# Kernel tuning notes

Measured on AMD Instinct MI355X. Metric: run time of the kernel, lower is better.

The kernel has to match this reference:

```python
import jax, jax.numpy as jnp
import numpy as np

# Model dims (match init_kwargs)
D_OUT = 64      # d_in == d_out
SEQ_L = 4096    # input_len
K_EIG = 24      # num_eigh
K_U = 3         # auto_reg_k_u
K_Y = 2         # auto_reg_k_y
BATCH = 8


def get_top_hankel_eigh(n, k):
    """Top-k eigenpairs of the Hankel matrix Z[i,j] = 2/((i+j)^3-(i+j)), 1-indexed."""
    idx = np.arange(1, n + 1, dtype=np.float64)
    s = idx[:, None] + idx[None, :]
    z = 2.0 / (s ** 3 - s)
    vals, vecs = np.linalg.eigh(z)  # ascending
    return (jnp.asarray(vals[-k:], jnp.float32),        # [k]
            jnp.asarray(vecs[:, -k:], jnp.float32))     # [n, k]


def setup_inputs() -> dict:
    key = jax.random.key(0)
    k1, k2, k3, k4 = jax.random.split(key, 4)
    eig_vals, eig_vecs = get_top_hankel_eigh(SEQ_L, K_EIG)
    m_x_var = 1.0 / float(D_OUT) ** 0.5
    return {
        "inputs": jax.random.normal(k1, (BATCH, SEQ_L, D_OUT), jnp.float32),
        "m_y": jax.random.normal(k2, (D_OUT, K_Y, D_OUT), jnp.float32) * 0.01,
        "m_u": jax.random.normal(k3, (D_OUT, D_OUT, K_U), jnp.float32) * m_x_var,
        "m_phi": jax.random.normal(k4, (D_OUT * K_EIG, D_OUT), jnp.float32) * 0.01,
        "eig_vals": eig_vals,
        "eig_vecs": eig_vecs,
    }


def _stu_single(x, m_y, m_u, m_phi, eig_vals, eig_vecs):
    """apply_stu for one sequence x: [L, d] -> [L, d]."""
    L, d = x.shape
    n = 2 * L
    # --- compute_x_tilde: causal FFT conv of each eigenvector with each channel ---
    V = jnp.fft.rfft(eig_vecs, n=n, axis=0)             # [F, k]
    U = jnp.fft.rfft(x, n=n, axis=0)                    # [F, d]
    xt = jnp.fft.irfft(V[:, :, None] * U[:, None, :], n=n, axis=0)[:L]  # [L, k, d]
    xt = xt * (eig_vals ** 0.25)[None, :, None]
    x_tilde = xt.reshape(L, K_EIG * d)                  # [L, k*d]
    # --- delta_phi ---
    delta_phi = jnp.einsum('lk,kd->ld', x_tilde, m_phi)  # [L, d_out]
    # --- compute_ar_x_preds: shifted AR input contributions ---
    o = jnp.einsum('oik,li->klo', m_u, x)               # [k_u, L, d_out]
    shifts = jnp.arange(K_U)
    o = jax.vmap(lambda a, i: jnp.roll(a, i, axis=0))(o, shifts)
    mask = (jnp.arange(L)[None, :] >= shifts[:, None]).astype(x.dtype)  # [k_u, L]
    delta_ar_u = jnp.sum(o * mask[:, :, None], axis=0)  # [L, d_out]
    deltas = delta_phi + delta_ar_u
    # --- compute_y_t: sequential AR recurrence over time ---
    def step(carry, dlt):  # carry: [k_y, d_out]
        out = jnp.tensordot(m_y, carry, axes=2) + dlt    # [d_out]
        carry = jnp.roll(carry, 1, axis=0).at[0].set(out)
        return carry, out
    _, ys = jax.lax.scan(step, jnp.zeros((K_Y, d), x.dtype), deltas)
    return ys  # [L, d_out]


def reference(inputs, m_y, m_u, m_phi, eig_vals, eig_vecs):
    return jax.vmap(lambda x: _stu_single(x, m_y, m_u, m_phi, eig_vals, eig_vecs))(inputs)
```

## Files before the change

kernel.cpp:

```cpp
#include <hip/hip_runtime.h>
#include <math.h>

#define BB 8
#define LL 4096
#define DD 64
#define KK 24
#define KT 27
#define NN 8192
#define LOGN 13
#define NP 4128
#define NCH 256
#define CH 16
#define PAD 80

typedef unsigned int uint;
typedef unsigned short u16;
typedef __attribute__((ext_vector_type(8))) short bf16x8;
typedef __attribute__((ext_vector_type(4))) float f32x4;

__device__ __forceinline__ float bfl(uint u) {
    union { uint u; float f; } v; v.u = u << 16; return v.f;
}
__device__ __forceinline__ float bfh(uint u) {
    union { uint u; float f; } v; v.u = u & 0xFFFF0000u; return v.f;
}
__device__ __forceinline__ uint pk(float x) {
    union { float f; uint u; } v; v.f = x;
    return (v.u + 0x7FFFu + ((v.u >> 16) & 1u)) >> 16;
}
__device__ __forceinline__ float2 unpk2(uint u) {
    return make_float2(bfl(u), bfh(u));
}
__device__ __forceinline__ int br13(int v) { return (int)(__brev((uint)v) >> 19); }

__global__ __launch_bounds__(512) void k_twiddle(float2* __restrict__ twc) {
    int i = blockIdx.x * 512 + threadIdx.x;
    if (i >= 8192) return;
    if (i == 0) { twc[0] = make_float2(1.f, 0.f); return; }
    int lh = 31 - __builtin_clz((uint)i);
    int j = i - (1 << lh);
    float ang = -6.28318530717958647692f * (float)j / (float)(2 << lh);
    float sn, cs;
    __sincosf(ang, &sn, &cs);
    twc[i] = make_float2(cs, sn);
}

template<int NT>
__device__ __forceinline__ void fft_dif(float2* a, const float2* __restrict__ twc) {
    const int tid = threadIdx.x;
    for (int lh = LOGN - 1; lh >= 0; --lh) {
        const int half = 1 << lh;
#pragma unroll
        for (int bb = 0; bb < NN / 2 / NT; ++bb) {
            int t = tid + bb * NT;
            int j = t & (half - 1);
            int i0 = ((t >> lh) << (lh + 1)) + j;
            float2 u = a[i0], v = a[i0 + half];
            float2 w = twc[half + j];
            float cs = w.x, sn = w.y;
            float dx = u.x - v.x, dy = u.y - v.y;
            a[i0] = make_float2(u.x + v.x, u.y + v.y);
            a[i0 + half] = make_float2(dx * cs - dy * sn, dx * sn + dy * cs);
        }
        __syncthreads();
    }
}

template<int NT>
__device__ __forceinline__ void fft_dit(float2* a, const float2* __restrict__ twc) {
    const int tid = threadIdx.x;
    for (int lh = 0; lh < LOGN; ++lh) {
        const int half = 1 << lh;
#pragma unroll
        for (int bb = 0; bb < NN / 2 / NT; ++bb) {
            int t = tid + bb * NT;
            int j = t & (half - 1);
            int i0 = ((t >> lh) << (lh + 1)) + j;
            float2 u = a[i0], v = a[i0 + half];
            float2 w = twc[half + j];
            float cs = w.x, sn = -w.y;
            float wx = v.x * cs - v.y * sn;
            float wy = v.x * sn + v.y * cs;
            a[i0] = make_float2(u.x + wx, u.y + wy);
            a[i0 + half] = make_float2(u.x - wx, u.y - wy);
        }
        __syncthreads();
    }
}


__global__ __launch_bounds__(256) void k_pack(const float* __restrict__ mphi,
                                              const float* __restrict__ mu,
                                              uint* __restrict__ mp2) {
    int idx = blockIdx.x * 256 + threadIdx.x;
    if (idx >= KT * 2048) return;
    int k = idx >> 11;
    int rem = idx & 2047;
    int o = rem >> 5, cp = rem & 31;
    int c = cp * 2;
    uint v;
    if (k < KK) {
        v = pk(mphi[(k * 64 + c) * 64 + o]) | (pk(mphi[(k * 64 + c + 1) * 64 + o]) << 16);
    } else {
        int ku = k - KK;
        v = pk(mu[(o * 64 + c) * 3 + ku]) | (pk(mu[(o * 64 + c + 1) * 3 + ku]) << 16);
    }
    mp2[idx] = v;
}

__global__ __launch_bounds__(256) void k_fft_filters(const float* __restrict__ eig_vals,
                                                     const float* __restrict__ eig_vecs,
                                                     const float2* __restrict__ twc,
                                                     float2* __restrict__ Vb) {
    __shared__ float2 a[NN];
    const int k = blockIdx.x, tid = threadIdx.x;
    const float alpha = powf(eig_vals[k], 0.25f) * (1.0f / (float)NN);
    for (int t = tid; t < LL; t += 256)
        a[t] = make_float2(eig_vecs[t * KK + k] * alpha, 0.f);
    for (int t = LL + tid; t < NN; t += 256)
        a[t] = make_float2(0.f, 0.f);
    __syncthreads();
    fft_dif<256>(a, twc);
    for (int r = tid; r < NN; r += 256)
        Vb[(size_t)r * KK + k] = a[r];
}

__global__ __launch_bounds__(512) void k_fft_x2(const float* __restrict__ x,
                                                const float2* __restrict__ twc,
                                                uint* __restrict__ Uxp,
                                                uint* __restrict__ Uyp) {
    __shared__ float2 a[NN];
    const int b = blockIdx.x & 7, cp = blockIdx.x >> 3;
    const int tid = threadIdx.x;
    for (int l = tid; l < LL; l += 512)
        a[l] = *(const float2*)&x[((size_t)b * LL + l) * DD + 2 * cp];
    for (int l = LL + tid; l < NN; l += 512)
        a[l] = make_float2(0.f, 0.f);
    __syncthreads();
    fft_dif<512>(a, twc);
    const size_t plane = ((size_t)b * 32 + cp) * NP;
    for (int idx = tid; idx < 4097; idx += 512) {
        int r = (idx == 4096) ? 1 : 2 * idx;
        int fn = br13(r);
        int q = br13((8192 - fn) & 8191);
        float2 Z = a[r], W = a[q];
        float ucx = 0.5f * (Z.x + W.x), ucy = 0.5f * (Z.y - W.y);
        float upx = 0.5f * (Z.y + W.y), upy = 0.5f * (W.x - Z.x);
        Uxp[plane + idx] = pk(ucx) | (pk(upx) << 16);
        Uyp[plane + idx] = pk(ucy) | (pk(upy) << 16);
    }
    for (int idx = 4097 + tid; idx < NP; idx += 512) {
        Uxp[plane + idx] = 0;
        Uyp[plane + idx] = 0;
    }
}

__global__ __launch_bounds__(256) void k_modulate5(const float2* __restrict__ Vb,
                                                   const uint* __restrict__ Uxp,
                                                   const uint* __restrict__ Uyp,
                                                   const uint* __restrict__ mp2,
                                                   uint* __restrict__ Sb2) {
    __shared__ u16 Uxs[32][PAD];
    __shared__ u16 Uys[32][PAD];
    __shared__ u16 mpT[2][64][PAD];
    __shared__ float2 Vt[32][28];
    const int tid = threadIdx.x;
    const int pt = blockIdx.x;
    const int b  = blockIdx.y;
    const int p0 = pt * 32;

    for (int i = tid; i < 1024; i += 256) {
        int cp = i >> 5, row = i & 31;
        uint vx = Uxp[((size_t)b * 32 + cp) * NP + p0 + row];
        uint vy = Uyp[((size_t)b * 32 + cp) * NP + p0 + row];
        *(uint*)&Uxs[row][cp * 2] = vx;
        *(uint*)&Uys[row][cp * 2] = vy;
    }
    {
        int o = tid >> 2, seg = tid & 3;
        const uint4* src = (const uint4*)&mp2[(size_t)o * 32 + seg * 8];
        uint4 m0 = src[0], m1 = src[1];
        *(uint4*)&mpT[0][o][seg * 16] = m0;
        *(uint4*)&mpT[0][o][seg * 16 + 8] = m1;
    }
    for (int i = tid; i < 768; i += 256) {
        int pi = i / 24, kk = i - pi * 24;
        int pidx = p0 + pi; if (pidx > 4096) pidx = 4096;
        int r = (pidx == 4096) ? 1 : 2 * pidx;
        Vt[pi][kk] = Vb[(size_t)r * KK + kk];
    }
    for (int pi = tid; pi < 32; pi += 256) {
        int pidx = p0 + pi; if (pidx > 4096) pidx = 4096;
        int r = (pidx == 4096) ? 1 : 2 * pidx;
        int f = br13(r);
        const float invN = 1.f / 8192.f;
        float ph = -6.28318530717958647692f * (float)f * invN;
        float s1, c1, s2, c2;
        __sincosf(ph, &s1, &c1);
        __sincosf(2.f * ph, &s2, &c2);
        Vt[pi][24] = make_float2(invN, 0.f);
        Vt[pi][25] = make_float2(c1 * invN, s1 * invN);
        Vt[pi][26] = make_float2(c2 * invN, s2 * invN);
    }
    __syncthreads();

    const int lane = tid & 63, w = tid >> 6;
    const int rt = w & 1, chalf = w >> 1;
    const int lrow = lane & 15, lk = lane >> 4;
    const u16* axp = &Uxs[rt * 16 + lrow][lk * 8];
    const u16* ayp = &Uys[rt * 16 + lrow][lk * 8];

    float Sx0[4] = {0.f, 0.f, 0.f, 0.f}, Sy0[4] = {0.f, 0.f, 0.f, 0.f};
    float Sx1[4] = {0.f, 0.f, 0.f, 0.f}, Sy1[4] = {0.f, 0.f, 0.f, 0.f};

    for (int k = 0; k < KT; ++k) {
        const int cur = k & 1;
        bf16x8 ax0 = *(const bf16x8*)(axp);
        bf16x8 ax1 = *(const bf16x8*)(axp + 32);
        bf16x8 ay0 = *(const bf16x8*)(ayp);
        bf16x8 ay1 = *(const bf16x8*)(ayp + 32);
        const u16* bp0 = &mpT[cur][chalf * 32 + lrow][lk * 8];
        const u16* bp1 = &mpT[cur][chalf * 32 + 16 + lrow][lk * 8];
        bf16x8 b00 = *(const bf16x8*)(bp0);
        bf16x8 b01 = *(const bf16x8*)(bp0 + 32);
        bf16x8 b10 = *(const bf16x8*)(bp1);
        bf16x8 b11 = *(const bf16x8*)(bp1 + 32);
        float2 v0 = Vt[rt * 16 + lk * 4 + 0][k];
        float2 v1 = Vt[rt * 16 + lk * 4 + 1][k];
        float2 v2 = Vt[rt * 16 + lk * 4 + 2][k];
        float2 v3 = Vt[rt * 16 + lk * 4 + 3][k];
        if (k + 1 < KT) {
            int o = tid >> 2, seg = tid & 3;
            const uint4* src = (const uint4*)&mp2[((size_t)(k + 1) * 64 + o) * 32 + seg * 8];
            uint4 m0 = src[0], m1 = src[1];
            *(uint4*)&mpT[cur ^ 1][o][seg * 16] = m0;
            *(uint4*)&mpT[cur ^ 1][o][seg * 16 + 8] = m1;
        }
        f32x4 z = {0.f, 0.f, 0.f, 0.f};
        f32x4 Wx0 = __builtin_amdgcn_mfma_f32_16x16x32_bf16(ax0, b00, z, 0, 0, 0);
        Wx0 = __builtin_amdgcn_mfma_f32_16x16x32_bf16(ax1, b01, Wx0, 0, 0, 0);
        f32x4 Wy0 = __builtin_amdgcn_mfma_f32_16x16x32_bf16(ay0, b00, z, 0, 0, 0);
        Wy0 = __builtin_amdgcn_mfma_f32_16x16x32_bf16(ay1, b01, Wy0, 0, 0, 0);
        f32x4 Wx1 = __builtin_amdgcn_mfma_f32_16x16x32_bf16(ax0, b10, z, 0, 0, 0);
        Wx1 = __builtin_amdgcn_mfma_f32_16x16x32_bf16(ax1, b11, Wx1, 0, 0, 0);
        f32x4 Wy1 = __builtin_amdgcn_mfma_f32_16x16x32_bf16(ay0, b10, z, 0, 0, 0);
        Wy1 = __builtin_amdgcn_mfma_f32_16x16x32_bf16(ay1, b11, Wy1, 0, 0, 0);
        Sx0[0] += v0.x * Wx0[0] - v0.y * Wy0[0];  Sy0[0] += v0.x * Wy0[0] + v0.y * Wx0[0];
        Sx0[1] += v1.x * Wx0[1] - v1.y * Wy0[1];  Sy0[1] += v1.x * Wy0[1] + v1.y * Wx0[1];
        Sx0[2] += v2.x * Wx0[2] - v2.y * Wy0[2];  Sy0[2] += v2.x * Wy0[2] + v2.y * Wx0[2];
        Sx0[3] += v3.x * Wx0[3] - v3.y * Wy0[3];  Sy0[3] += v3.x * Wy0[3] + v3.y * Wx0[3];
        Sx1[0] += v0.x * Wx1[0] - v0.y * Wy1[0];  Sy1[0] += v0.x * Wy1[0] + v0.y * Wx1[0];
        Sx1[1] += v1.x * Wx1[1] - v1.y * Wy1[1];  Sy1[1] += v1.x * Wy1[1] + v1.y * Wx1[1];
        Sx1[2] += v2.x * Wx1[2] - v2.y * Wy1[2];  Sy1[2] += v2.x * Wy1[2] + v2.y * Wx1[2];
        Sx1[3] += v3.x * Wx1[3] - v3.y * Wy1[3];  Sy1[3] += v3.x * Wy1[3] + v3.y * Wx1[3];
        __syncthreads();
    }
    const int rbase = rt * 16 + lk * 4;
    const int o0 = chalf * 32 + lrow;
    const size_t pl0 = ((size_t)b * 64 + o0) * NP + p0 + rbase;
    const size_t pl1 = ((size_t)b * 64 + o0 + 16) * NP + p0 + rbase;
#pragma unroll
    for (int j = 0; j < 4; ++j) {
        Sb2[pl0 + j] = pk(Sx0[j]) | (pk(Sy0[j]) << 16);
        Sb2[pl1 + j] = pk(Sx1[j]) | (pk(Sy1[j]) << 16);
    }
}

__global__ __launch_bounds__(512) void k_ifft2(const uint* __restrict__ Sb2,
                                               const float2* __restrict__ twc,
                                               float* __restrict__ deltas) {
    __shared__ float2 a[NN];
    const int b = blockIdx.x & 7, op = blockIdx.x >> 3;
    const int tid = threadIdx.x;
    const uint* s0 = &Sb2[((size_t)b * 64 + op * 2) * NP];
    const uint* s1 = &Sb2[((size_t)b * 64 + op * 2 + 1) * NP];
    for (int idx = tid; idx < 4097; idx += 512) {
        int r = (idx == 4096) ? 1 : 2 * idx;
        float2 A = unpk2(s0[idx]), B = unpk2(s1[idx]);
        a[r] = make_float2(A.x - B.y, A.y + B.x);
        int fn = br13(r);
        int q = br13((8192 - fn) & 8191);
        if (q != r) a[q] = make_float2(A.x + B.y, B.x - A.y);
    }
    __syncthreads();
    fft_dit<512>(a, twc);
    float* d0 = &deltas[((size_t)b * 64 + op * 2) * LL];
    float* d1 = &deltas[((size_t)b * 64 + op * 2 + 1) * LL];
    for (int l = tid; l < LL; l += 512) {
        d0[l] = a[l].x;
        d1[l] = a[l].y;
    }
}

__global__ __launch_bounds__(256) void k_matsq1(const float* __restrict__ m_y,
                                                float* __restrict__ C) {
    int idx = blockIdx.x * 256 + threadIdx.x;
    int r = idx >> 7, c = idx & 127;
    if (r >= 64) { C[idx] = m_y[(r - 64) * 128 + c]; return; }
    float acc = (c < 64) ? m_y[r * 128 + 64 + c] : 0.f;
#pragma unroll
    for (int i = 0; i < 64; ++i) acc += m_y[r * 128 + i] * m_y[i * 128 + c];
    C[idx] = acc;
}

__global__ __launch_bounds__(256) void k_matsq(const float* __restrict__ A,
                                               float* __restrict__ C) {
    int idx = blockIdx.x * 256 + threadIdx.x;
    int r = idx >> 7, c = idx & 127;
    float acc = 0.f;
#pragma unroll
    for (int i = 0; i < 128; ++i) acc += A[r * 128 + i] * A[i * 128 + c];
    C[idx] = acc;
}

__device__ __forceinline__ void load_rowhalf(const float* __restrict__ P, int r, int h,
                                             float* __restrict__ p) {
#pragma unroll
    for (int i4 = 0; i4 < 16; ++i4) {
        float4 v = *(const float4*)&P[r * 128 + h * 64 + i4 * 4];
        p[4 * i4] = v.x; p[4 * i4 + 1] = v.y; p[4 * i4 + 2] = v.z; p[4 * i4 + 3] = v.w;
    }
}
__device__ __forceinline__ float dot64(const float* __restrict__ p, const float* s) {
    float a0 = 0.f, a1 = 0.f, a2 = 0.f, a3 = 0.f;
#pragma unroll
    for (int i4 = 0; i4 < 16; ++i4) {
        float4 w = *(const float4*)&s[i4 * 4];
        a0 += p[4 * i4] * w.x;  a1 += p[4 * i4 + 1] * w.y;
        a2 += p[4 * i4 + 2] * w.z;  a3 += p[4 * i4 + 3] * w.w;
    }
    return (a0 + a1) + (a2 + a3);
}

__global__ __launch_bounds__(256, 1) void k_scan(const float* __restrict__ P,
                                                 const float* __restrict__ in,
                                                 float* __restrict__ partial,
                                                 float* __restrict__ terminal,
                                                 const int count) {
    const int bx = blockIdx.x;
    const int tid = threadIdx.x;
    const int r = tid & 127, h = tid >> 7;
    __shared__ __align__(16) float scur[128];
    __shared__ float pacc[256];
    float p[64];
    load_rowhalf(P, r, h, p);
    if (tid < 128) scur[tid] = 0.f;
    __syncthreads();
    const size_t base = (size_t)bx * count * 128;
    for (int k = 0; k < count; ++k) {
        if (tid < 128) partial[base + (size_t)k * 128 + tid] = scur[tid];
        pacc[tid] = dot64(p, &scur[h * 64]);
        __syncthreads();
        if (tid < 128) scur[tid] = pacc[tid] + pacc[tid + 128] + in[base + (size_t)k * 128 + tid];
        __syncthreads();
    }
    if (tid < 128) terminal[(size_t)bx * 128 + tid] = scur[tid];
}

__global__ __launch_bounds__(256, 1) void k_fixupg(const float* __restrict__ P,
                                                   const float* __restrict__ Sinit,
                                                   const float* __restrict__ q,
                                                   float* __restrict__ out,
                                                   const int count) {
    const int bx = blockIdx.x;
    const int tid = threadIdx.x;
    const int r = tid & 127, h = tid >> 7;
    __shared__ __align__(16) float scur[128];
    __shared__ float pacc[256];
    float p[64];
    load_rowhalf(P, r, h, p);
    if (tid < 128) scur[tid] = Sinit[(size_t)bx * 128 + tid];
    __syncthreads();
    const size_t base = (size_t)bx * count * 128;
    for (int k = 0; k < count; ++k) {
        if (tid < 128) out[base + (size_t)k * 128 + tid] = scur[tid] + q[base + (size_t)k * 128 + tid];
        if (k == count - 1) break;
        pacc[tid] = dot64(p, &scur[h * 64]);
        __syncthreads();
        if (tid < 128) scur[tid] = pacc[tid] + pacc[tid + 128];
        __syncthreads();
    }
}

__global__ __launch_bounds__(128, 1) void k_chunk_local(const float* __restrict__ deltas,
                                                        const float* __restrict__ m_y,
                                                        float* __restrict__ term) {
    const int b = blockIdx.x >> 8, j = blockIdx.x & 255;
    const int tid = threadIdx.x;
    const int o = tid & 63, h = tid >> 6;
    __shared__ __align__(16) float y1s[64];
    __shared__ __align__(16) float y2s[64];
    __shared__ float pacc[128];
    float m1[32], m2[32];
#pragma unroll
    for (int i4 = 0; i4 < 8; ++i4) {
        float4 v1 = *(const float4*)&m_y[o * 128 + h * 32 + i4 * 4];
        float4 v2 = *(const float4*)&m_y[o * 128 + 64 + h * 32 + i4 * 4];
        m1[4 * i4] = v1.x; m1[4 * i4 + 1] = v1.y; m1[4 * i4 + 2] = v1.z; m1[4 * i4 + 3] = v1.w;
        m2[4 * i4] = v2.x; m2[4 * i4 + 1] = v2.y; m2[4 * i4 + 2] = v2.z; m2[4 * i4 + 3] = v2.w;
    }
    if (tid < 64) { y1s[tid] = 0.f; y2s[tid] = 0.f; }
    __syncthreads();
    const float* dl = &deltas[((size_t)b * 64 + o) * LL + j * CH];
    for (int t = 0; t < CH; ++t) {
        float a0 = 0.f, a1 = 0.f, a2 = 0.f, a3 = 0.f;
#pragma unroll
        for (int i4 = 0; i4 < 8; ++i4) {
            float4 w1 = *(const float4*)&y1s[h * 32 + i4 * 4];
            float4 w2 = *(const float4*)&y2s[h * 32 + i4 * 4];
            a0 += m1[4 * i4] * w1.x + m2[4 * i4] * w2.x;
            a1 += m1[4 * i4 + 1] * w1.y + m2[4 * i4 + 1] * w2.y;
            a2 += m1[4 * i4 + 2] * w1.z + m2[4 * i4 + 2] * w2.z;
            a3 += m1[4 * i4 + 3] * w1.w + m2[4 * i4 + 3] * w2.w;
        }
        pacc[tid] = (a0 + a1) + (a2 + a3);
        __syncthreads();
        if (h == 0) {
            float outv = pacc[o] + pacc[o + 64] + dl[t];
            y2s[o] = y1s[o];
            y1s[o] = outv;
        }
        __syncthreads();
    }
    if (tid < 64) {
        term[((size_t)b * NCH + j) * 128 + o] = y1s[o];
        term[((size_t)b * NCH + j) * 128 + 64 + o] = y2s[o];
    }
}

__global__ __launch_bounds__(128, 1) void k_chunk_final(const float* __restrict__ deltas,
                                                        const float* __restrict__ m_y,
                                                        const float* __restrict__ sstate,
                                                        float* __restrict__ out) {
    const int b = blockIdx.x >> 8, j = blockIdx.x & 255;
    const int tid = threadIdx.x;
    const int o = tid & 63, h = tid >> 6;
    __shared__ __align__(16) float y1s[64];
    __shared__ __align__(16) float y2s[64];
    __shared__ float pacc[128];
    float m1[32], m2[32];
#pragma unroll
    for (int i4 = 0; i4 < 8; ++i4) {
        float4 v1 = *(const float4*)&m_y[o * 128 + h * 32 + i4 * 4];
        float4 v2 = *(const float4*)&m_y[o * 128 + 64 + h * 32 + i4 * 4];
        m1[4 * i4] = v1.x; m1[4 * i4 + 1] = v1.y; m1[4 * i4 + 2] = v1.z; m1[4 * i4 + 3] = v1.w;
        m2[4 * i4] = v2.x; m2[4 * i4 + 1] = v2.y; m2[4 * i4 + 2] = v2.z; m2[4 * i4 + 3] = v2.w;
    }
    if (tid < 64) {
        y1s[tid] = sstate[((size_t)b * NCH + j) * 128 + tid];
        y2s[tid] = sstate[((size_t)b * NCH + j) * 128 + 64 + tid];
    }
    __syncthreads();
    const float* dl = &deltas[((size_t)b * 64 + o) * LL + j * CH];
    const size_t obase = (((size_t)b * LL) + j * CH) * DD + o;
    for (int t = 0; t < CH; ++t) {
        float a0 = 0.f, a1 = 0.f, a2 = 0.f, a3 = 0.f;
#pragma unroll
        for (int i4 = 0; i4 < 8; ++i4) {
            float4 w1 = *(const float4*)&y1s[h * 32 + i4 * 4];
            float4 w2 = *(const float4*)&y2s[h * 32 + i4 * 4];
            a0 += m1[4 * i4] * w1.x + m2[4 * i4] * w2.x;
            a1 += m1[4 * i4 + 1] * w1.y + m2[4 * i4 + 1] * w2.y;
            a2 += m1[4 * i4 + 2] * w1.z + m2[4 * i4 + 2] * w2.z;
            a3 += m1[4 * i4 + 3] * w1.w + m2[4 * i4 + 3] * w2.w;
        }
        pacc[tid] = (a0 + a1) + (a2 + a3);
        __syncthreads();
        if (h == 0) {
            float outv = pacc[o] + pacc[o + 64] + dl[t];
            out[obase + (size_t)t * DD] = outv;
            y2s[o] = y1s[o];
            y1s[o] = outv;
        }
        __syncthreads();
    }
}

extern "C" void kernel_launch(void* const* d_in, const int* in_sizes, int n_in,
                              void* d_out, int out_size, void* d_ws, size_t ws_size,
                              hipStream_t stream) {
    const float* x        = (const float*)d_in[0];
    const float* m_y      = (const float*)d_in[1];
    const float* m_u      = (const float*)d_in[2];
    const float* m_phi    = (const float*)d_in[3];
    const float* eig_vals = (const float*)d_in[4];
    const float* eig_vecs = (const float*)d_in[5];
    float* out = (float*)d_out;

    char* ws = (char*)d_ws;
    size_t off = 0;
    auto alloc = [&](size_t bytes) -> void* {
        void* p = ws + off;
        off += (bytes + 255) & ~(size_t)255;
        return p;
    };
    float2* Vb   = (float2*)alloc((size_t)NN * KK * sizeof(float2));
    uint*   Uxp  = (uint*)alloc((size_t)BB * 32 * NP * sizeof(uint));
    uint*   Uyp  = (uint*)alloc((size_t)BB * 32 * NP * sizeof(uint));
    uint*   Sb2  = (uint*)alloc((size_t)BB * 64 * NP * sizeof(uint));
    float*  deltas = (float*)alloc((size_t)BB * 64 * LL * sizeof(float));
    uint*   mp2  = (uint*)alloc((size_t)KT * 64 * 32 * sizeof(uint));
    float2* twcg = (float2*)alloc((size_t)8192 * sizeof(float2));
    float*  mats = (float*)alloc((size_t)4 * 128 * 128 * sizeof(float));
    float*  term = (float*)alloc((size_t)BB * NCH * 128 * sizeof(float));
    float*  sst  = (float*)alloc((size_t)BB * NCH * 128 * sizeof(float));
    float*  qbuf = (float*)alloc((size_t)BB * NCH * 128 * sizeof(float));
    float*  Qg   = (float*)alloc((size_t)BB * 16 * 128 * sizeof(float));
    float*  Sgt  = (float*)alloc((size_t)BB * 16 * 128 * sizeof(float));
    float*  dmy  = (float*)alloc((size_t)8 * 128 * sizeof(float));

    k_twiddle<<<dim3(16), dim3(512), 0, stream>>>(twcg);
    k_pack<<<dim3(216), dim3(256), 0, stream>>>(m_phi, m_u, mp2);
    k_fft_filters<<<dim3(24), dim3(256), 0, stream>>>(eig_vals, eig_vecs, twcg, Vb);
    k_fft_x2<<<dim3(256), dim3(512), 0, stream>>>(x, twcg, Uxp, Uyp);

    float* T1   = mats;
    float* T2   = mats + 16384;
    float* P16  = mats + 32768;
    float* P256 = mats + 49152;
    k_matsq1<<<dim3(64), dim3(256), 0, stream>>>(m_y, T1);
    k_matsq<<<dim3(64), dim3(256), 0, stream>>>(T1, T2);
    k_matsq<<<dim3(64), dim3(256), 0, stream>>>(T2, T1);
    k_matsq<<<dim3(64), dim3(256), 0, stream>>>(T1, P16);
    k_matsq<<<dim3(64), dim3(256), 0, stream>>>(P16, T1);
    k_matsq<<<dim3(64), dim3(256), 0, stream>>>(T1, T2);
    k_matsq<<<dim3(64), dim3(256), 0, stream>>>(T2, T1);
    k_matsq<<<dim3(64), dim3(256), 0, stream>>>(T1, P256);

    k_modulate5<<<dim3(129, 8), dim3(256), 0, stream>>>(Vb, Uxp, Uyp, mp2, Sb2);
    k_ifft2<<<dim3(256), dim3(512), 0, stream>>>(Sb2, twcg, deltas);

    k_chunk_local<<<dim3(2048), dim3(128), 0, stream>>>(deltas, m_y, term);
    k_scan<<<dim3(128), dim3(256), 0, stream>>>(P16, term, qbuf, Qg, 16);
    k_scan<<<dim3(8), dim3(256), 0, stream>>>(P256, Qg, Sgt, dmy, 16);
    k_fixupg<<<dim3(128), dim3(256), 0, stream>>>(P16, Sgt, qbuf, sst, 16);
    k_chunk_final<<<dim3(2048), dim3(128), 0, stream>>>(deltas, m_y, sst, out);
}
```

Before: 240.7 us.

## Split modulation into two launches with whole weight slabs preloaded into LDS

The modulation kernel is split into two launches, each covering about half of the 27 weight slabs. Each launch loads all of its slabs into shared memory up front, which removes the per-iteration __syncthreads and double-buffered refill. The U fragments are also hoisted out of the loop. The cost is larger LDS usage (about 143 KB per block, likely one block per CU), a second launch, and a bf16 read-modify-write of Sb2 that adds rounding error and extra global traffic.

New measurement: 315.6 us. 31.1% more time.

```diff
diff --git a/kernel.cpp b/kernel.cpp
--- a/kernel.cpp
+++ b/kernel.cpp
@@ -12,6 +12,7 @@
 #define NCH 256
 #define CH 16
 #define PAD 80
+#define NKMAX 14
 
 typedef unsigned int uint;
 typedef unsigned short u16;
@@ -155,20 +156,28 @@
     }
 }
 
-__global__ __launch_bounds__(256) void k_modulate5(const float2* __restrict__ Vb,
+__global__ __launch_bounds__(256) void k_modulate7(const float2* __restrict__ Vb,
                                                    const uint* __restrict__ Uxp,
                                                    const uint* __restrict__ Uyp,
                                                    const uint* __restrict__ mp2,
-                                                   uint* __restrict__ Sb2) {
-    __shared__ u16 Uxs[32][PAD];
-    __shared__ u16 Uys[32][PAD];
-    __shared__ u16 mpT[2][64][PAD];
-    __shared__ float2 Vt[32][28];
+                                                   uint* __restrict__ Sb2,
+                                                   const int k0, const int nk,
+                                                   const int accum) {
+    __shared__ u16 mpT[NKMAX][64][PAD];
+    __shared__ u16 Uxs[32][72];
+    __shared__ u16 Uys[32][72];
+    __shared__ float2 Vt[32][NKMAX];
     const int tid = threadIdx.x;
     const int pt = blockIdx.x;
     const int b  = blockIdx.y;
     const int p0 = pt * 32;
 
+    for (int i = tid; i < nk * 512; i += 256) {
+        int slab = i >> 9, e = i & 511;
+        int o = e >> 3, seg = e & 7;
+        uint4 m = ((const uint4*)&mp2[((size_t)(k0 + slab) * 64 + o) * 32])[seg];
+        *(uint4*)&mpT[slab][o][seg * 8] = m;
+    }
     for (int i = tid; i < 1024; i += 256) {
         int cp = i >> 5, row = i & 31;
         uint vx = Uxp[((size_t)b * 32 + cp) * NP + p0 + row];
@@ -176,31 +185,21 @@
         *(uint*)&Uxs[row][cp * 2] = vx;
         *(uint*)&Uys[row][cp * 2] = vy;
     }
-    {
-        int o = tid >> 2, seg = tid & 3;
-        const uint4* src = (const uint4*)&mp2[(size_t)o * 32 + seg * 8];
-        uint4 m0 = src[0], m1 = src[1];
-        *(uint4*)&mpT[0][o][seg * 16] = m0;
-        *(uint4*)&mpT[0][o][seg * 16 + 8] = m1;
-    }
-    for (int i = tid; i < 768; i += 256) {
-        int pi = i / 24, kk = i - pi * 24;
+    for (int i = tid; i < 32 * nk; i += 256) {
+        int pi = i / nk, kk = i - pi * nk;
+        int kg = k0 + kk;
         int pidx = p0 + pi; if (pidx > 4096) pidx = 4096;
         int r = (pidx == 4096) ? 1 : 2 * pidx;
-        Vt[pi][kk] = Vb[(size_t)r * KK + kk];
-    }
-    for (int pi = tid; pi < 32; pi += 256) {
-        int pidx = p0 + pi; if (pidx > 4096) pidx = 4096;
-        int r = (pidx == 4096) ? 1 : 2 * pidx;
-        int f = br13(r);
-        const float invN = 1.f / 8192.f;
-        float ph = -6.28318530717958647692f * (float)f * invN;
-        float s1, c1, s2, c2;
-        __sincosf(ph, &s1, &c1);
-        __sincosf(2.f * ph, &s2, &c2);
-        Vt[pi][24] = make_float2(invN, 0.f);
-        Vt[pi][25] = make_float2(c1 * invN, s1 * invN);
-        Vt[pi][26] = make_float2(c2 * invN, s2 * invN);
+        if (kg < KK) {
+            Vt[pi][kk] = Vb[(size_t)r * KK + kg];
+        } else {
+            int f = br13(r);
+            const float invN = 1.f / 8192.f;
+            float ph = -6.28318530717958647692f * (float)f * invN * (float)(kg - KK);
+            float sn, cs;
+            __sincosf(ph, &sn, &cs);
+            Vt[pi][kk] = make_float2(cs * invN, sn * invN);
+        }
     }
     __syncthreads();
 
@@ -209,33 +208,25 @@
     const int lrow = lane & 15, lk = lane >> 4;
     const u16* axp = &Uxs[rt * 16 + lrow][lk * 8];
     const u16* ayp = &Uys[rt * 16 + lrow][lk * 8];
+    bf16x8 ax0 = *(const bf16x8*)(axp);
+    bf16x8 ax1 = *(const bf16x8*)(axp + 32);
+    bf16x8 ay0 = *(const bf16x8*)(ayp);
+    bf16x8 ay1 = *(const bf16x8*)(ayp + 32);
 
     float Sx0[4] = {0.f, 0.f, 0.f, 0.f}, Sy0[4] = {0.f, 0.f, 0.f, 0.f};
     float Sx1[4] = {0.f, 0.f, 0.f, 0.f}, Sy1[4] = {0.f, 0.f, 0.f, 0.f};
 
-    for (int k = 0; k < KT; ++k) {
-        const int cur = k & 1;
-        bf16x8 ax0 = *(const bf16x8*)(axp);
-        bf16x8 ax1 = *(const bf16x8*)(axp + 32);
-        bf16x8 ay0 = *(const bf16x8*)(ayp);
-        bf16x8 ay1 = *(const bf16x8*)(ayp + 32);
-        const u16* bp0 = &mpT[cur][chalf * 32 + lrow][lk * 8];
-        const u16* bp1 = &mpT[cur][chalf * 32 + 16 + lrow][lk * 8];
+    for (int kk = 0; kk < nk; ++kk) {
+        const u16* bp0 = &mpT[kk][chalf * 32 + lrow][lk * 8];
+        const u16* bp1 = &mpT[kk][chalf * 32 + 16 + lrow][lk * 8];
         bf16x8 b00 = *(const bf16x8*)(bp0);
         bf16x8 b01 = *(const bf16x8*)(bp0 + 32);
         bf16x8 b10 = *(const bf16x8*)(bp1);
         bf16x8 b11 = *(const bf16x8*)(bp1 + 32);
-        float2 v0 = Vt[rt * 16 + lk * 4 + 0][k];
-        float2 v1 = Vt[rt * 16 + lk * 4 + 1][k];
-        float2 v2 = Vt[rt * 16 + lk * 4 + 2][k];
-        float2 v3 = Vt[rt * 16 + lk * 4 + 3][k];
-        if (k + 1 < KT) {
-            int o = tid >> 2, seg = tid & 3;
-            const uint4* src = (const uint4*)&mp2[((size_t)(k + 1) * 64 + o) * 32 + seg * 8];
-            uint4 m0 = src[0], m1 = src[1];
-            *(uint4*)&mpT[cur ^ 1][o][seg * 16] = m0;
-            *(uint4*)&mpT[cur ^ 1][o][seg * 16 + 8] = m1;
-        }
+        float2 v0 = Vt[rt * 16 + lk * 4 + 0][kk];
+        float2 v1 = Vt[rt * 16 + lk * 4 + 1][kk];
+        float2 v2 = Vt[rt * 16 + lk * 4 + 2][kk];
+        float2 v3 = Vt[rt * 16 + lk * 4 + 3][kk];
         f32x4 z = {0.f, 0.f, 0.f, 0.f};
         f32x4 Wx0 = __builtin_amdgcn_mfma_f32_16x16x32_bf16(ax0, b00, z, 0, 0, 0);
         Wx0 = __builtin_amdgcn_mfma_f32_16x16x32_bf16(ax1, b01, Wx0, 0, 0, 0);
@@ -253,12 +244,19 @@
         Sx1[1] += v1.x * Wx1[1] - v1.y * Wy1[1];  Sy1[1] += v1.x * Wy1[1] + v1.y * Wx1[1];
         Sx1[2] += v2.x * Wx1[2] - v2.y * Wy1[2];  Sy1[2] += v2.x * Wy1[2] + v2.y * Wx1[2];
         Sx1[3] += v3.x * Wx1[3] - v3.y * Wy1[3];  Sy1[3] += v3.x * Wy1[3] + v3.y * Wx1[3];
-        __syncthreads();
     }
     const int rbase = rt * 16 + lk * 4;
     const int o0 = chalf * 32 + lrow;
     const size_t pl0 = ((size_t)b * 64 + o0) * NP + p0 + rbase;
     const size_t pl1 = ((size_t)b * 64 + o0 + 16) * NP + p0 + rbase;
+    if (accum) {
+#pragma unroll
+        for (int j = 0; j < 4; ++j) {
+            uint old0 = Sb2[pl0 + j], old1 = Sb2[pl1 + j];
+            Sx0[j] += bfl(old0); Sy0[j] += bfh(old0);
+            Sx1[j] += bfl(old1); Sy1[j] += bfh(old1);
+        }
+    }
 #pragma unroll
     for (int j = 0; j < 4; ++j) {
         Sb2[pl0 + j] = pk(Sx0[j]) | (pk(Sy0[j]) << 16);
@@ -527,7 +525,8 @@
     k_matsq<<<dim3(64), dim3(256), 0, stream>>>(T2, T1);
     k_matsq<<<dim3(64), dim3(256), 0, stream>>>(T1, P256);
 
-    k_modulate5<<<dim3(129, 8), dim3(256), 0, stream>>>(Vb, Uxp, Uyp, mp2, Sb2);
+    k_modulate7<<<dim3(129, 8), dim3(256), 0, stream>>>(Vb, Uxp, Uyp, mp2, Sb2, 0, 13, 0);
+    k_modulate7<<<dim3(129, 8), dim3(256), 0, stream>>>(Vb, Uxp, Uyp, mp2, Sb2, 13, 14, 1);
     k_ifft2<<<dim3(256), dim3(512), 0, stream>>>(Sb2, twcg, deltas);
 
     k_chunk_local<<<dim3(2048), dim3(128), 0, stream>>>(deltas, m_y, term);
```
